# Kernel optimization log

Hardware: AMD Instinct MI355X
Metric: run time of the kernel (lower is better)

## Reference

```python
import jax, jax.numpy as jnp
import numpy as np

EPS = 1e-5  # torch BatchNorm default eps


def _bn(x, gamma, beta, axes):
    # training-mode batch norm over `axes` (channel axis is 1), biased variance as in torch
    mean = x.mean(axis=axes, keepdims=True)
    var = x.var(axis=axes, keepdims=True)
    shp = [1] * x.ndim
    shp[1] = -1
    return gamma.reshape(shp) * (x - mean) * jax.lax.rsqrt(var + EPS) + beta.reshape(shp)


def setup_inputs() -> dict:
    key = jax.random.key(0)
    k0, k1, k2 = jax.random.split(key, 3)
    B, C, H, W = 4, 64, 128, 128
    OP2 = 128      # out_planes * 2
    HEAD = 8       # head_dim
    HP = OP2 // HEAD  # head_planes = 16
    return {
        "x": jax.random.normal(k0, (B, C, H, W), jnp.float32),
        "w_qkv": jax.random.normal(k1, (OP2, C), jnp.float32) / np.sqrt(C).astype(np.float32),
        "gamma1": jnp.ones((OP2,), jnp.float32),
        "beta1": jnp.zeros((OP2,), jnp.float32),
        "pos_relative": jax.random.normal(k2, (HP, 2 * H - 1), jnp.float32) / np.sqrt(C).astype(np.float32),
        "gate_qr": jnp.array([0.1], jnp.float32),
        "gate_kr": jnp.array([0.1], jnp.float32),
        "gate_v_pos": jnp.array([0.1], jnp.float32),
        "gate_v": jnp.array([1.0], jnp.float32),
        "gamma_att": jnp.ones((3 * HEAD,), jnp.float32),
        "beta_att": jnp.zeros((3 * HEAD,), jnp.float32),
        "gamma_v": jnp.ones((2 * HEAD,), jnp.float32),
        "beta_v": jnp.zeros((2 * HEAD,), jnp.float32),
    }


def reference(x, w_qkv, gamma1, beta1, pos_relative, gate_qr, gate_kr,
              gate_v_pos, gate_v, gamma_att, beta_att, gamma_v, beta_v):
    b, c, H, W = x.shape
    # h_w='h': permute [0,3,1,2] -> (b, W, c, H), fuse (b, W)
    xp = jnp.transpose(x, (0, 3, 1, 2)).reshape(b * W, c, H)  # [N, c, H]
    # to_qkv: 1x1 Conv1d (no bias) + ReLU + BatchNorm1d (training mode)
    y = jax.nn.relu(jnp.einsum('oc,ncl->nol', w_qkv, xp))      # [N, 2*out_planes, H]
    y = _bn(y, gamma1, beta1, (0, 2))

    head_dim = gamma_att.shape[0] // 3
    hp = y.shape[1] // head_dim          # head_planes
    qk_dim = hp // 4
    v_dim = hp // 2
    qkv = y.reshape(-1, head_dim, hp, H)  # [N, head_dim, head_planes, H]
    q = qkv[:, :, :qk_dim]
    k = qkv[:, :, qk_dim:2 * qk_dim]
    v = qkv[:, :, 2 * qk_dim:]

    # relative-position gather: pos_relative[:, q_idx - k_idx + H - 1] -> [head_planes, H, H]
    rel = jnp.arange(H)[:, None] - jnp.arange(H)[None, :] + H - 1
    qk_pos = pos_relative[:, rel]
    q_pos = qk_pos[:qk_dim]
    k_pos = qk_pos[qk_dim:2 * qk_dim]
    v_pos = qk_pos[2 * qk_dim:]

    qk = jnp.einsum('nhcp,nhci->nhpi', q, k)                 # [N, head_dim, H, H]
    qr = jnp.einsum('nhcp,cpi->nhpi', q, q_pos) * gate_qr
    kr = jnp.einsum('nhcp,cpi->nhpi', k, k_pos) * gate_kr

    att = _bn(jnp.concatenate([qk, qr, kr], axis=1), gamma_att, beta_att, (0, 2, 3))
    att = att.reshape(-1, 3, head_dim, H, H).sum(axis=1)
    att = jax.nn.softmax(att, axis=-1)

    att_v = jnp.einsum('nhpi,nhci->nhcp', att, v * gate_v)          # [N, head_dim, v_dim, H]
    att_vp = jnp.einsum('nhpi,cpi->nhcp', att, v_pos * gate_v_pos)

    z = _bn(jnp.concatenate([att_v, att_vp], axis=1), gamma_v, beta_v, (0, 2, 3))
    z = z.reshape(b, W, 2, head_dim * v_dim, H).sum(axis=2)  # [b, W, out_planes, H]
    # h_w='h': permute [0,2,3,1] -> (b, out_planes, H, W)
    return jnp.transpose(z, (0, 2, 3, 1))
```

## Files before the change

### kernel.cpp

```cpp
#include <hip/hip_runtime.h>
#include <hip/hip_fp16.h>

#define EPS 1e-5f



typedef _Float16 half2_t __attribute__((ext_vector_type(2)));

__device__ __constant__ int pair_c [10] = {0,0,0,0,1,1,1,2,2,3};
__device__ __constant__ int pair_cp[10] = {0,1,2,3,1,2,3,2,3,3};
__device__ __constant__ int s_base[6] = {512, 536, 520, 544, 528, 552};

__device__ inline float fdot2(half2_t a, half2_t b, float c) {
#if __has_builtin(__builtin_amdgcn_fdot2)
  return __builtin_amdgcn_fdot2(a, b, c, false);
#else
  return c + (float)a[0] * (float)b[0] + (float)a[1] * (float)b[1];
#endif
}
__device__ inline half2_t bch2(unsigned u) {
  union { unsigned u; half2_t h; } x; x.u = u; return x.h;
}
__device__ inline unsigned packf2(float a, float b) {
  half2_t h; h[0] = (_Float16)a; h[1] = (_Float16)b;
  union { unsigned u; half2_t h; } x; x.h = h; return x.u;
}

__global__ __launch_bounds__(256) void k1_gemm(
    const float* __restrict__ x, const float* __restrict__ wq,
    float* __restrict__ y1, float* __restrict__ Pbuf)
{
  __shared__ float xs[64][132];
  const int b = blockIdx.x >> 7, l = blockIdx.x & 127;
  const int tid = threadIdx.x;
  const float* xp = x + (size_t)b * 1048576 + (size_t)l * 128;
  for (int idx = tid; idx < 8192; idx += 256) {
    int c = idx >> 7, wv = idx & 127;
    xs[c][wv] = xp[c * 16384 + wv];
  }
  __syncthreads();
  const int ty = tid >> 4, tx = tid & 15;
  const int o0 = ty * 8, w0 = tx * 4;
  float acc[8][8];
#pragma unroll
  for (int u = 0; u < 8; ++u)
#pragma unroll
    for (int v = 0; v < 8; ++v) acc[u][v] = 0.f;

  for (int c4 = 0; c4 < 64; c4 += 4) {
    float wr[8][4];
#pragma unroll
    for (int u = 0; u < 8; ++u)
      *(float4*)&wr[u][0] = *(const float4*)&wq[(o0 + u) * 64 + c4];
#pragma unroll
    for (int dc = 0; dc < 4; ++dc) {
      float4 xa = *(const float4*)&xs[c4 + dc][w0];
      float4 xb = *(const float4*)&xs[c4 + dc][w0 + 64];
#pragma unroll
      for (int u = 0; u < 8; ++u) {
        float wv = wr[u][dc];
        acc[u][0] += wv * xa.x; acc[u][1] += wv * xa.y;
        acc[u][2] += wv * xa.z; acc[u][3] += wv * xa.w;
        acc[u][4] += wv * xb.x; acc[u][5] += wv * xb.y;
        acc[u][6] += wv * xb.z; acc[u][7] += wv * xb.w;
      }
    }
  }
  float* y1p = y1 + (size_t)(b * 128 + l) * 16384;
#pragma unroll
  for (int u = 0; u < 8; ++u) {
#pragma unroll
    for (int v = 0; v < 8; ++v) acc[u][v] = fmaxf(acc[u][v], 0.f);
    float4 r0 = make_float4(acc[u][0], acc[u][1], acc[u][2], acc[u][3]);
    float4 r1 = make_float4(acc[u][4], acc[u][5], acc[u][6], acc[u][7]);
    *(float4*)&y1p[(o0 + u) * 128 + w0] = r0;
    *(float4*)&y1p[(o0 + u) * 128 + w0 + 64] = r1;
    float s  = acc[u][0] + acc[u][1] + acc[u][2] + acc[u][3]
             + acc[u][4] + acc[u][5] + acc[u][6] + acc[u][7];
    float ss = acc[u][0]*acc[u][0] + acc[u][1]*acc[u][1] + acc[u][2]*acc[u][2]
             + acc[u][3]*acc[u][3] + acc[u][4]*acc[u][4] + acc[u][5]*acc[u][5]
             + acc[u][6]*acc[u][6] + acc[u][7]*acc[u][7];
#pragma unroll
    for (int off = 1; off < 16; off <<= 1) {
      s  += __shfl_xor(s, off);
      ss += __shfl_xor(ss, off);
    }
    if (tx == 0) {
      Pbuf[blockIdx.x * 256 + o0 + u] = s;
      Pbuf[blockIdx.x * 256 + 128 + o0 + u] = ss;
    }
  }
}

__global__ __launch_bounds__(64) void k2_bn1(
    const float* __restrict__ Pbuf, float* __restrict__ S,
    const float* __restrict__ g1, const float* __restrict__ b1)
{
  const int t = blockIdx.x;
  const int lane = threadIdx.x;
  float s1 = 0.f, s2 = 0.f;
#pragma unroll
  for (int m = 0; m < 8; ++m) {
    int blk = lane + 64 * m;
    s1 += Pbuf[blk * 256 + t];
    s2 += Pbuf[blk * 256 + 128 + t];
  }
#pragma unroll
  for (int off = 1; off < 64; off <<= 1) {
    s1 += __shfl_xor(s1, off);
    s2 += __shfl_xor(s2, off);
  }
  if (lane == 0) {
    const float inv = 1.f / 65536.f;
    float m = s1 * inv;
    float var = s2 * inv - m * m;
    float sc = g1[t] * rsqrtf(var + EPS);
    S[256 + t] = sc;
    S[384 + t] = b1[t] - m * sc;
  }
}

__global__ __launch_bounds__(256) void k_tr(
    const float* __restrict__ y1, const float* __restrict__ S,
    unsigned* __restrict__ y2h)
{
  __shared__ _Float16 th[2][64][134];
  const int s = blockIdx.x & 63, b = blockIdx.x >> 6;
  const int h = s >> 3, slot = s & 7;
  const int o0 = 2 * s, o1 = 2 * s + 1;
  const float sc0 = S[256 + o0], sh0 = S[384 + o0];
  const float sc1 = S[256 + o1], sh1 = S[384 + o1];
  const int tid = threadIdx.x;
  for (int lh = 0; lh < 2; ++lh) {
    const int l0 = lh * 64;
    for (int idx = tid; idx < 8192; idx += 256) {
      int ll = idx >> 7, w = idx & 127;
      size_t base = ((size_t)(b * 128 + l0 + ll) * 128) * 128 + w;
      float v0 = y1[base + (size_t)o0 * 128];
      float v1 = y1[base + (size_t)o1 * 128];
      th[0][ll][w] = (_Float16)(v0 * sc0 + sh0);
      th[1][ll][w] = (_Float16)(v1 * sc1 + sh1);
    }
    __syncthreads();
    for (int idx = tid; idx < 8192; idx += 256) {
      int w = idx >> 6, ll = idx & 63;
      unsigned pk;
      { half2_t hh; hh[0] = th[0][ll][w]; hh[1] = th[1][ll][w];
        union { unsigned u; half2_t h; } xx; xx.h = hh; pk = xx.u; }
      y2h[((size_t)((b * 128 + w) * 8 + h) * 8 + slot) * 128 + l0 + ll] = pk;
    }
    __syncthreads();
  }
}

__global__ __launch_bounds__(128) void k0_pos(const float* __restrict__ pos,
                                              float* __restrict__ PT,
                                              unsigned* __restrict__ pos_h)
{
  const int blk = blockIdx.x, tid = threadIdx.x;
  if (blk == 28) {
    for (int u = tid; u < 255; u += 128) {
#pragma unroll
      for (int s = 0; s < 12; ++s) {
        unsigned val = 0;
        if (s < 8) val = packf2(pos[(2 * s) * 255 + u], pos[(2 * s + 1) * 255 + u]);
        pos_h[u * 12 + s] = val;
      }
    }
    return;
  }
  __shared__ float r0[255], r1[255];
  int rowA, rowB, out;
  bool prod;
  if (blk < 4)       { rowA = blk;                 rowB = rowA;               out = blk * 128;              prod = false; }
  else if (blk < 14) { int m = blk - 4;  rowA = pair_c[m];     rowB = pair_cp[m];     out = 1024 + m * 128; prod = true; }
  else if (blk < 18) { rowA = 4 + (blk - 14);      rowB = rowA;               out = 512 + (blk - 14) * 128; prod = false; }
  else               { int m = blk - 18; rowA = 4 + pair_c[m]; rowB = 4 + pair_cp[m]; out = 2304 + m * 128; prod = true; }
  for (int u = tid; u < 255; u += 128) {
    r0[u] = pos[rowA * 255 + u];
    r1[u] = pos[rowB * 255 + u];
  }
  __syncthreads();
  float s = 0.f;
  if (prod) {
    for (int d = 0; d < 128; ++d) s += r0[tid + d] * r1[tid + d];
  } else {
    for (int d = 0; d < 128; ++d) s += r0[tid + d];
  }
  PT[out + tid] = s;
}

__global__ __launch_bounds__(256) void k3_stats(
    const unsigned* __restrict__ y2h, const float* __restrict__ PT,
    float* __restrict__ Pb3)
{
  const int W = blockIdx.x * 4 + (threadIdx.x >> 6);
  const int lane = threadIdx.x & 63;
  const int h = W & 7;
  const int n0 = (W >> 3) * 8;
  float Pq[4][2], Pk[4][2], Wq[10][2], Wk[10][2];
#pragma unroll
  for (int c = 0; c < 4; ++c) {
    Pq[c][0] = PT[c * 128 + lane];        Pq[c][1] = PT[c * 128 + 64 + lane];
    Pk[c][0] = PT[512 + c * 128 + lane];  Pk[c][1] = PT[512 + c * 128 + 64 + lane];
  }
#pragma unroll
  for (int m = 0; m < 10; ++m) {
    Wq[m][0] = PT[1024 + m * 128 + lane]; Wq[m][1] = PT[1024 + m * 128 + 64 + lane];
    Wk[m][0] = PT[2304 + m * 128 + lane]; Wk[m][1] = PT[2304 + m * 128 + 64 + lane];
  }
  float acc_qk = 0, acc_qkss = 0, acc_qr = 0, acc_qrss = 0, acc_kr = 0, acc_krss = 0;
  for (int t = 0; t < 8; ++t) {
    const unsigned* yb = y2h + (size_t)((n0 + t) * 8 + h) * 1024;
    float q[4][2], k[4][2];
#pragma unroll
    for (int pl = 0; pl < 2; ++pl) {
      half2_t ha = bch2(yb[pl * 128 + lane]);
      half2_t hb = bch2(yb[pl * 128 + 64 + lane]);
      q[2 * pl][0] = (float)ha[0]; q[2 * pl + 1][0] = (float)ha[1];
      q[2 * pl][1] = (float)hb[0]; q[2 * pl + 1][1] = (float)hb[1];
      half2_t hc = bch2(yb[(2 + pl) * 128 + lane]);
      half2_t hd = bch2(yb[(2 + pl) * 128 + 64 + lane]);
      k[2 * pl][0] = (float)hc[0]; k[2 * pl + 1][0] = (float)hc[1];
      k[2 * pl][1] = (float)hd[0]; k[2 * pl + 1][1] = (float)hd[1];
    }
#pragma unroll
    for (int c = 0; c < 4; ++c) {
      acc_qr += q[c][0] * Pq[c][0] + q[c][1] * Pq[c][1];
      acc_kr += k[c][0] * Pk[c][0] + k[c][1] * Pk[c][1];
    }
#pragma unroll
    for (int m = 0; m < 10; ++m) {
      int c = pair_c[m], cp = pair_cp[m];
      float mult = (c == cp) ? 1.f : 2.f;
      acc_qrss += mult * (q[c][0] * q[cp][0] * Wq[m][0] + q[c][1] * q[cp][1] * Wq[m][1]);
      acc_krss += mult * (k[c][0] * k[cp][0] * Wk[m][0] + k[c][1] * k[cp][1] * Wk[m][1]);
    }
    float vals[28];
#pragma unroll
    for (int c = 0; c < 4; ++c) {
      vals[c]     = q[c][0] + q[c][1];
      vals[4 + c] = k[c][0] + k[c][1];
    }
#pragma unroll
    for (int m = 0; m < 10; ++m) {
      int c = pair_c[m], cp = pair_cp[m];
      vals[8 + m]  = q[c][0] * q[cp][0] + q[c][1] * q[cp][1];
      vals[18 + m] = k[c][0] * k[cp][0] + k[c][1] * k[cp][1];
    }
#pragma unroll
    for (int v = 0; v < 28; ++v) {
      float tv = vals[v];
#pragma unroll
      for (int off = 1; off < 64; off <<= 1) tv += __shfl_xor(tv, off);
      vals[v] = tv;
    }
    float qk = 0, qkss = 0;
#pragma unroll
    for (int c = 0; c < 4; ++c) qk += vals[c] * vals[4 + c];
#pragma unroll
    for (int m = 0; m < 10; ++m) {
      float mult = (pair_c[m] == pair_cp[m]) ? 1.f : 2.f;
      qkss += mult * vals[8 + m] * vals[18 + m];
    }
    acc_qk += qk; acc_qkss += qkss;
  }
  float lin[4] = {acc_qr, acc_qrss, acc_kr, acc_krss};
#pragma unroll
  for (int v = 0; v < 4; ++v) {
    float tv = lin[v];
#pragma unroll
    for (int off = 1; off < 64; off <<= 1) tv += __shfl_xor(tv, off);
    lin[v] = tv;
  }
  if (lane == 0) {
    float* o = Pb3 + W * 6;
    o[0] = acc_qk; o[1] = acc_qkss;
    o[2] = lin[0]; o[3] = lin[1]; o[4] = lin[2]; o[5] = lin[3];
  }
}

__global__ __launch_bounds__(64) void k3_red(
    const float* __restrict__ Pb3, float* __restrict__ S)
{
  const int h = blockIdx.x / 6, k = blockIdx.x % 6;
  const int g = threadIdx.x;
  float v = Pb3[(h + 8 * g) * 6 + k];
#pragma unroll
  for (int off = 1; off < 64; off <<= 1) v += __shfl_xor(v, off);
  if (g == 0) S[s_base[k] + h] = v;
}

__global__ void k4_att(float* __restrict__ S, const float* __restrict__ ga,
                       const float* __restrict__ ba,
                       const float* __restrict__ gqr, const float* __restrict__ gkr)
{
  int h = threadIdx.x;
  if (h >= 8) return;
  const float inv = 1.f / 8388608.f;
  float gates[3] = {1.f, gqr[0], gkr[0]};
  float csum = 0.f;
#pragma unroll
  for (int g = 0; g < 3; ++g) {
    float mr = S[512 + g * 8 + h] * inv;
    float er = S[536 + g * 8 + h] * inv;
    float gt = gates[g];
    float mean = gt * mr;
    float var = gt * gt * er - mean * mean;
    float sc = ga[g * 8 + h] * rsqrtf(var + EPS);
    S[560 + g * 8 + h] = gt * sc;
    csum += ba[g * 8 + h] - mean * sc;
  }
  S[584 + h] = csum;
}

__global__ __launch_bounds__(512, 6) void k5_apply(
    const unsigned* __restrict__ y2h, const unsigned* __restrict__ pos_h,
    float* __restrict__ S, _Float16* __restrict__ av, _Float16* __restrict__ avp,
    const float* __restrict__ gv_p, const float* __restrict__ gvp_p,
    float* __restrict__ Vbuf)
{
  __shared__ __align__(16) unsigned qkv_s[128][8];
  __shared__ __align__(16) unsigned posm[255][12];
  __shared__ float red[8][4];
  const int h = blockIdx.x & 7, n = blockIdx.x >> 3;
  const int tid = threadIdx.x;
  const unsigned* yb = y2h + (size_t)(n * 8 + h) * 1024;
  unsigned* qf = (unsigned*)qkv_s;
  for (int m = tid; m < 1024; m += 512)
    qf[m] = yb[(m & 7) * 128 + (m >> 3)];
  unsigned* pf = (unsigned*)posm;
  for (int m = tid; m < 3060; m += 512) pf[m] = pos_h[m];
  __syncthreads();

  const int p = tid >> 2, isub = tid & 3;
  uint4 qk4 = *(const uint4*)&qkv_s[p][0];
  const half2_t q01 = bch2(qk4.x), q23 = bch2(qk4.y);
  const half2_t k01 = bch2(qk4.z), k23 = bch2(qk4.w);
  const float C0 = S[560 + h], C1 = S[568 + h], C2 = S[576 + h], C3v = S[584 + h];

  float sum = 0.f;
  float accv[8], accvp[8];
#pragma unroll
  for (int c = 0; c < 8; ++c) { accv[c] = 0.f; accvp[c] = 0.f; }

#pragma unroll 4
  for (int j = 0; j < 32; ++j) {
    int i = isub + 4 * j;
    int u = p - i + 127;
    uint2 kt  = *(const uint2*)&qkv_s[i][2];
    uint4 qkp = *(const uint4*)&posm[u][0];
    float aa = fdot2(q23, bch2(kt.y),  fdot2(q01, bch2(kt.x),  0.f));
    float bq = fdot2(q23, bch2(qkp.y), fdot2(q01, bch2(qkp.x), 0.f));
    float ck = fdot2(k23, bch2(qkp.w), fdot2(k01, bch2(qkp.z), 0.f));
    float s = aa * C0 + bq * C1 + ck * C2 + C3v;
    float e = __expf(s - 9.f);
    sum += e;
    uint4 vv = *(const uint4*)&qkv_s[i][4];
    uint4 vp = *(const uint4*)&posm[u][4];
    half2_t v0 = bch2(vv.x), v1 = bch2(vv.y), v2 = bch2(vv.z), v3 = bch2(vv.w);
    half2_t w0 = bch2(vp.x), w1 = bch2(vp.y), w2 = bch2(vp.z), w3 = bch2(vp.w);
    accv[0] += e * (float)v0[0]; accv[1] += e * (float)v0[1];
    accv[2] += e * (float)v1[0]; accv[3] += e * (float)v1[1];
    accv[4] += e * (float)v2[0]; accv[5] += e * (float)v2[1];
    accv[6] += e * (float)v3[0]; accv[7] += e * (float)v3[1];
    accvp[0] += e * (float)w0[0]; accvp[1] += e * (float)w0[1];
    accvp[2] += e * (float)w1[0]; accvp[3] += e * (float)w1[1];
    accvp[4] += e * (float)w2[0]; accvp[5] += e * (float)w2[1];
    accvp[6] += e * (float)w3[0]; accvp[7] += e * (float)w3[1];
  }
  sum += __shfl_xor(sum, 1);
  sum += __shfl_xor(sum, 2);
#pragma unroll
  for (int c = 0; c < 8; ++c) {
    accv[c]  += __shfl_xor(accv[c], 1);  accv[c]  += __shfl_xor(accv[c], 2);
    accvp[c] += __shfl_xor(accvp[c], 1); accvp[c] += __shfl_xor(accvp[c], 2);
  }

  float sv = 0, ssv = 0, svp = 0, ssvp = 0;
  if (isub == 0) {
    const float fv = gv_p[0] / sum, fp2 = gvp_p[0] / sum;
    size_t base = ((size_t)(n * 8 + h) * 8) * 128 + p;
#pragma unroll
    for (int c = 0; c < 8; ++c) {
      float x1 = accv[c] * fv;
      float x2 = accvp[c] * fp2;
      av [base + c * 128] = (_Float16)x1;
      avp[base + c * 128] = (_Float16)x2;
      sv += x1; ssv += x1 * x1; svp += x2; ssvp += x2 * x2;
    }
  }
  float vals[4] = {sv, ssv, svp, ssvp};
#pragma unroll
  for (int kk = 0; kk < 4; ++kk) {
    float v = vals[kk];
#pragma unroll
    for (int off = 1; off < 64; off <<= 1) v += __shfl_xor(v, off);
    vals[kk] = v;
  }
  const int wid = tid >> 6, lane = tid & 63;
  if (lane == 0) {
#pragma unroll
    for (int kk = 0; kk < 4; ++kk) red[wid][kk] = vals[kk];
  }
  __syncthreads();
  if (tid == 0) {
    float t0 = 0, t1 = 0, t2 = 0, t3 = 0;
#pragma unroll
    for (int w = 0; w < 8; ++w) {
      t0 += red[w][0]; t1 += red[w][1]; t2 += red[w][2]; t3 += red[w][3];
    }
    float* o = Vbuf + (size_t)blockIdx.x * 4;
    o[0] = t0; o[1] = t1; o[2] = t2; o[3] = t3;
  }
}

__global__ __launch_bounds__(64) void k6_red(
    const float* __restrict__ Vbuf, float* __restrict__ S)
{
  const int k = blockIdx.x >> 3, h = blockIdx.x & 7;
  const int lane = threadIdx.x;
  float v = 0.f;
#pragma unroll
  for (int j = 0; j < 8; ++j) {
    int n = lane + 64 * j;
    v += Vbuf[(size_t)(n * 8 + h) * 4 + k];
  }
#pragma unroll
  for (int off = 1; off < 64; off <<= 1) v += __shfl_xor(v, off);
  if (lane == 0) {
    const int dst[4] = {592, 608, 600, 616};
    S[dst[k] + h] = v;
  }
}

__global__ void k6_v(float* __restrict__ S, const float* __restrict__ gv,
                     const float* __restrict__ bv)
{
  int h = threadIdx.x;
  if (h >= 8) return;
  const float inv = 1.f / 524288.f;
  float m = S[592 + h] * inv;
  float var = S[608 + h] * inv - m * m;
  float sc = gv[h] * rsqrtf(var + EPS);
  S[624 + h] = sc;
  S[632 + h] = bv[h] - m * sc;
  m = S[600 + h] * inv;
  var = S[616 + h] * inv - m * m;
  sc = gv[8 + h] * rsqrtf(var + EPS);
  S[640 + h] = sc;
  S[648 + h] = bv[8 + h] - m * sc;
}

__global__ __launch_bounds__(256) void k7_out(
    const _Float16* __restrict__ av, const _Float16* __restrict__ avp,
    const float* __restrict__ S, float* __restrict__ out)
{
  __shared__ float tile[64][129];
  const int wt = blockIdx.x & 1;
  const int d  = (blockIdx.x >> 1) & 63;
  const int b  = blockIdx.x >> 7;
  const int h = d >> 3, c = d & 7;
  const float scv = S[624 + h], shv = S[632 + h];
  const float scp = S[640 + h], shp = S[648 + h];
  const int tid = threadIdx.x;
  for (int idx = tid; idx < 8192; idx += 256) {
    int wl = idx >> 7, p = idx & 127;
    int n = b * 128 + wt * 64 + wl;
    size_t base = (((size_t)n * 8 + h) * 8 + c) * 128 + p;
    tile[wl][p] = (float)av[base] * scv + shv + (float)avp[base] * scp + shp;
  }
  __syncthreads();
  for (int idx = tid; idx < 8192; idx += 256) {
    int p = idx >> 6, wl = idx & 63;
    out[(((size_t)b * 64 + d) * 128 + p) * 128 + wt * 64 + wl] = tile[wl][p];
  }
}

extern "C" void kernel_launch(void* const* d_in, const int* in_sizes, int n_in,
                              void* d_out, int out_size, void* d_ws, size_t ws_size,
                              hipStream_t stream)
{
  const float* x   = (const float*)d_in[0];
  const float* wq  = (const float*)d_in[1];
  const float* g1  = (const float*)d_in[2];
  const float* b1  = (const float*)d_in[3];
  const float* pos = (const float*)d_in[4];
  const float* gqr = (const float*)d_in[5];
  const float* gkr = (const float*)d_in[6];
  const float* gvp = (const float*)d_in[7];
  const float* gv  = (const float*)d_in[8];
  const float* ga  = (const float*)d_in[9];
  const float* ba  = (const float*)d_in[10];
  const float* gv2 = (const float*)d_in[11];
  const float* bv2 = (const float*)d_in[12];

  float* ws = (float*)d_ws;
  float*    y1    = ws;
  _Float16* av    = (_Float16*)ws;
  _Float16* avp   = (_Float16*)ws + 4194304;
  float*    Pb3   = ws + 4200000;
  float*    Vbuf  = ws + 4250000;
  float*    Pbuf  = ws + 8388608;
  unsigned* y2h   = (unsigned*)(ws + 8388608);
  float*    S     = ws + 16777216;
  unsigned* pos_h = (unsigned*)(ws + 16778240);
  float*    PT    = ws + 16781312;
  float*    out   = (float*)d_out;

  hipMemsetAsync(S, 0, 1024 * sizeof(float), stream);
  k0_pos<<<29, 128, 0, stream>>>(pos, PT, pos_h);
  k1_gemm<<<512, 256, 0, stream>>>(x, wq, y1, Pbuf);
  k2_bn1<<<128, 64, 0, stream>>>(Pbuf, S, g1, b1);
  k_tr<<<256, 256, 0, stream>>>(y1, S, y2h);
  k3_stats<<<128, 256, 0, stream>>>(y2h, PT, Pb3);
  k3_red<<<48, 64, 0, stream>>>(Pb3, S);
  k4_att<<<1, 64, 0, stream>>>(S, ga, ba, gqr, gkr);
  k5_apply<<<4096, 512, 0, stream>>>(y2h, pos_h, S, av, avp, gv, gvp, Vbuf);
  k6_red<<<32, 64, 0, stream>>>(Vbuf, S);
  k6_v<<<1, 64, 0, stream>>>(S, gv2, bv2);
  k7_out<<<512, 256, 0, stream>>>(av, avp, S, out);
}
```

Measured before the change: 218.4 us.

## Store conv output in fp16, fuse small reductions, pack softmax-V dots with online max

The 1x1-conv output is now written as fp16 instead of fp32, which halves traffic between the GEMM and the transpose kernel. The tiny reduction and BN-coefficient kernels are merged (k3_red+k4_att into kR1, k6_red+k6_v into kR2) and the memset is dropped, which removes several launches. The attention-apply kernel now processes key pairs with packed fp16 exp weights and fdot2 for the V and V-pos accumulation. It uses an online running max in place of a fixed offset, with a pre-transposed V tile and a precomputed reversed v_pos table. This lowers ALU and LDS work, at the cost of extra fp16 rounding of y1 and of the exp weights.

```diff
diff --git a/kernel.cpp b/kernel.cpp
--- a/kernel.cpp
+++ b/kernel.cpp
@@ -9,7 +9,6 @@
 
 __device__ __constant__ int pair_c [10] = {0,0,0,0,1,1,1,2,2,3};
 __device__ __constant__ int pair_cp[10] = {0,1,2,3,1,2,3,2,3,3};
-__device__ __constant__ int s_base[6] = {512, 536, 520, 544, 528, 552};
 
 __device__ inline float fdot2(half2_t a, half2_t b, float c) {
 #if __has_builtin(__builtin_amdgcn_fdot2)
@@ -28,7 +27,7 @@
 
 __global__ __launch_bounds__(256) void k1_gemm(
     const float* __restrict__ x, const float* __restrict__ wq,
-    float* __restrict__ y1, float* __restrict__ Pbuf)
+    _Float16* __restrict__ y1h, float* __restrict__ Pbuf)
 {
   __shared__ float xs[64][132];
   const int b = blockIdx.x >> 7, l = blockIdx.x & 127;
@@ -66,15 +65,16 @@
       }
     }
   }
-  float* y1p = y1 + (size_t)(b * 128 + l) * 16384;
+  _Float16* y1p = y1h + (size_t)(b * 128 + l) * 16384;
 #pragma unroll
   for (int u = 0; u < 8; ++u) {
 #pragma unroll
     for (int v = 0; v < 8; ++v) acc[u][v] = fmaxf(acc[u][v], 0.f);
-    float4 r0 = make_float4(acc[u][0], acc[u][1], acc[u][2], acc[u][3]);
-    float4 r1 = make_float4(acc[u][4], acc[u][5], acc[u][6], acc[u][7]);
-    *(float4*)&y1p[(o0 + u) * 128 + w0] = r0;
-    *(float4*)&y1p[(o0 + u) * 128 + w0 + 64] = r1;
+    uint2 pa, pb;
+    pa.x = packf2(acc[u][0], acc[u][1]); pa.y = packf2(acc[u][2], acc[u][3]);
+    pb.x = packf2(acc[u][4], acc[u][5]); pb.y = packf2(acc[u][6], acc[u][7]);
+    *(uint2*)&y1p[(o0 + u) * 128 + w0] = pa;
+    *(uint2*)&y1p[(o0 + u) * 128 + w0 + 64] = pb;
     float s  = acc[u][0] + acc[u][1] + acc[u][2] + acc[u][3]
              + acc[u][4] + acc[u][5] + acc[u][6] + acc[u][7];
     float ss = acc[u][0]*acc[u][0] + acc[u][1]*acc[u][1] + acc[u][2]*acc[u][2]
@@ -121,7 +121,7 @@
 }
 
 __global__ __launch_bounds__(256) void k_tr(
-    const float* __restrict__ y1, const float* __restrict__ S,
+    const _Float16* __restrict__ y1h, const float* __restrict__ S,
     unsigned* __restrict__ y2h)
 {
   __shared__ _Float16 th[2][64][134];
@@ -133,13 +133,16 @@
   const int tid = threadIdx.x;
   for (int lh = 0; lh < 2; ++lh) {
     const int l0 = lh * 64;
-    for (int idx = tid; idx < 8192; idx += 256) {
-      int ll = idx >> 7, w = idx & 127;
-      size_t base = ((size_t)(b * 128 + l0 + ll) * 128) * 128 + w;
-      float v0 = y1[base + (size_t)o0 * 128];
-      float v1 = y1[base + (size_t)o1 * 128];
-      th[0][ll][w] = (_Float16)(v0 * sc0 + sh0);
-      th[1][ll][w] = (_Float16)(v1 * sc1 + sh1);
+    for (int idx = tid; idx < 4096; idx += 256) {
+      int ll = idx >> 6, wp = idx & 63;
+      size_t base = ((size_t)(b * 128 + l0 + ll) * 128) * 128 + 2 * wp;
+      unsigned a0 = *(const unsigned*)&y1h[base + (size_t)o0 * 128];
+      unsigned a1 = *(const unsigned*)&y1h[base + (size_t)o1 * 128];
+      half2_t ha = bch2(a0), hb = bch2(a1);
+      *(unsigned*)&th[0][ll][2 * wp] =
+          packf2((float)ha[0] * sc0 + sh0, (float)ha[1] * sc0 + sh0);
+      *(unsigned*)&th[1][ll][2 * wp] =
+          packf2((float)hb[0] * sc1 + sh1, (float)hb[1] * sc1 + sh1);
     }
     __syncthreads();
     for (int idx = tid; idx < 8192; idx += 256) {
@@ -155,17 +158,30 @@
 
 __global__ __launch_bounds__(128) void k0_pos(const float* __restrict__ pos,
                                               float* __restrict__ PT,
-                                              unsigned* __restrict__ pos_h)
+                                              unsigned* __restrict__ pos_h,
+                                              unsigned* __restrict__ vpxg)
 {
   const int blk = blockIdx.x, tid = threadIdx.x;
   if (blk == 28) {
     for (int u = tid; u < 255; u += 128) {
 #pragma unroll
-      for (int s = 0; s < 12; ++s) {
-        unsigned val = 0;
-        if (s < 8) val = packf2(pos[(2 * s) * 255 + u], pos[(2 * s + 1) * 255 + u]);
-        pos_h[u * 12 + s] = val;
+      for (int s = 0; s < 4; ++s)
+        pos_h[u * 4 + s] = packf2(pos[(2 * s) * 255 + u], pos[(2 * s + 1) * 255 + u]);
+    }
+    return;
+  }
+  if (blk == 29) {
+    for (int m = tid; m < 3072; m += 128) {
+      int sel = m / 1536, rem = m % 1536, rp = rem / 12, c = rem % 12;
+      unsigned val = 0;
+      if (c < 8) {
+        int ua = (sel ? 254 : 253) - 2 * rp;
+        int ub = ua - 1;
+        float fa = (ua >= 0) ? pos[(8 + c) * 255 + ua] : 0.f;
+        float fb = (ub >= 0) ? pos[(8 + c) * 255 + ub] : 0.f;
+        val = packf2(fa, fb);
       }
+      vpxg[m] = val;
     }
     return;
   }
@@ -280,94 +296,148 @@
   }
 }
 
-__global__ __launch_bounds__(64) void k3_red(
-    const float* __restrict__ Pb3, float* __restrict__ S)
-{
-  const int h = blockIdx.x / 6, k = blockIdx.x % 6;
-  const int g = threadIdx.x;
-  float v = Pb3[(h + 8 * g) * 6 + k];
-#pragma unroll
-  for (int off = 1; off < 64; off <<= 1) v += __shfl_xor(v, off);
-  if (g == 0) S[s_base[k] + h] = v;
-}
-
-__global__ void k4_att(float* __restrict__ S, const float* __restrict__ ga,
-                       const float* __restrict__ ba,
-                       const float* __restrict__ gqr, const float* __restrict__ gkr)
-{
-  int h = threadIdx.x;
-  if (h >= 8) return;
-  const float inv = 1.f / 8388608.f;
-  float gates[3] = {1.f, gqr[0], gkr[0]};
-  float csum = 0.f;
-#pragma unroll
-  for (int g = 0; g < 3; ++g) {
-    float mr = S[512 + g * 8 + h] * inv;
-    float er = S[536 + g * 8 + h] * inv;
-    float gt = gates[g];
-    float mean = gt * mr;
-    float var = gt * gt * er - mean * mean;
-    float sc = ga[g * 8 + h] * rsqrtf(var + EPS);
-    S[560 + g * 8 + h] = gt * sc;
-    csum += ba[g * 8 + h] - mean * sc;
-  }
-  S[584 + h] = csum;
+__global__ __launch_bounds__(64) void kR1(
+    const float* __restrict__ Pb3, float* __restrict__ S,
+    const float* __restrict__ ga, const float* __restrict__ ba,
+    const float* __restrict__ gqr, const float* __restrict__ gkr)
+{
+  __shared__ float sums[48];
+  const int t = threadIdx.x;
+  if (t < 48) {
+    int h = t / 6, k = t % 6;
+    float v = 0.f;
+    for (int g = 0; g < 64; ++g) v += Pb3[(h + 8 * g) * 6 + k];
+    sums[t] = v;
+  }
+  __syncthreads();
+  if (t < 8) {
+    const int h = t;
+    const float inv = 1.f / 8388608.f;
+    float gates[3] = {1.f, gqr[0], gkr[0]};
+    float csum = 0.f;
+#pragma unroll
+    for (int g = 0; g < 3; ++g) {
+      float mr = sums[h * 6 + 2 * g] * inv;
+      float er = sums[h * 6 + 2 * g + 1] * inv;
+      float gt = gates[g];
+      float mean = gt * mr;
+      float var = gt * gt * er - mean * mean;
+      float sc = ga[g * 8 + h] * rsqrtf(var + EPS);
+      S[560 + g * 8 + h] = gt * sc;
+      csum += ba[g * 8 + h] - mean * sc;
+    }
+    S[584 + h] = csum;
+  }
 }
 
 __global__ __launch_bounds__(512, 6) void k5_apply(
     const unsigned* __restrict__ y2h, const unsigned* __restrict__ pos_h,
+    const unsigned* __restrict__ vpxg,
     float* __restrict__ S, _Float16* __restrict__ av, _Float16* __restrict__ avp,
     const float* __restrict__ gv_p, const float* __restrict__ gvp_p,
     float* __restrict__ Vbuf)
 {
-  __shared__ __align__(16) unsigned qkv_s[128][8];
-  __shared__ __align__(16) unsigned posm[255][12];
+  __shared__ __align__(16) unsigned qkv_s[128][4];
+  __shared__ __align__(16) unsigned posm[255][4];
+  __shared__ __align__(16) unsigned vt[64][8];
+  __shared__ __align__(16) unsigned vpx[2][128][12];
   __shared__ float red[8][4];
   const int h = blockIdx.x & 7, n = blockIdx.x >> 3;
   const int tid = threadIdx.x;
   const unsigned* yb = y2h + (size_t)(n * 8 + h) * 1024;
-  unsigned* qf = (unsigned*)qkv_s;
-  for (int m = tid; m < 1024; m += 512)
-    qf[m] = yb[(m & 7) * 128 + (m >> 3)];
-  unsigned* pf = (unsigned*)posm;
-  for (int m = tid; m < 3060; m += 512) pf[m] = pos_h[m];
+  {
+    int l = tid >> 2, s = tid & 3;
+    qkv_s[l][s] = yb[s * 128 + l];
+  }
+  {
+    unsigned* pf = (unsigned*)posm;
+    for (int m = tid; m < 1020; m += 512) pf[m] = pos_h[m];
+  }
+  {
+    unsigned* pf = (unsigned*)vpx;
+    for (int m = tid; m < 3072; m += 512) pf[m] = vpxg[m];
+  }
+  if (tid < 256) {
+    int s = tid & 3, jp = tid >> 2;
+    unsigned a0 = yb[(4 + s) * 128 + 2 * jp];
+    unsigned a1 = yb[(4 + s) * 128 + 2 * jp + 1];
+    vt[jp][2 * s]     = (a0 & 0xffffu) | (a1 << 16);
+    vt[jp][2 * s + 1] = (a0 >> 16) | (a1 & 0xffff0000u);
+  }
   __syncthreads();
 
   const int p = tid >> 2, isub = tid & 3;
-  uint4 qk4 = *(const uint4*)&qkv_s[p][0];
-  const half2_t q01 = bch2(qk4.x), q23 = bch2(qk4.y);
-  const half2_t k01 = bch2(qk4.z), k23 = bch2(qk4.w);
+  uint2 qk2 = *(const uint2*)&qkv_s[p][0];
+  uint2 kown = *(const uint2*)&qkv_s[p][2];
+  const half2_t q01 = bch2(qk2.x), q23 = bch2(qk2.y);
+  const half2_t k01o = bch2(kown.x), k23o = bch2(kown.y);
   const float C0 = S[560 + h], C1 = S[568 + h], C2 = S[576 + h], C3v = S[584 + h];
-
+  const unsigned* vprow = &vpx[p & 1][63 - (p >> 1)][0];
+
+  float mcur = -1e30f;
   float sum = 0.f;
   float accv[8], accvp[8];
 #pragma unroll
   for (int c = 0; c < 8; ++c) { accv[c] = 0.f; accvp[c] = 0.f; }
 
 #pragma unroll 4
-  for (int j = 0; j < 32; ++j) {
-    int i = isub + 4 * j;
-    int u = p - i + 127;
-    uint2 kt  = *(const uint2*)&qkv_s[i][2];
-    uint4 qkp = *(const uint4*)&posm[u][0];
-    float aa = fdot2(q23, bch2(kt.y),  fdot2(q01, bch2(kt.x),  0.f));
-    float bq = fdot2(q23, bch2(qkp.y), fdot2(q01, bch2(qkp.x), 0.f));
-    float ck = fdot2(k23, bch2(qkp.w), fdot2(k01, bch2(qkp.z), 0.f));
-    float s = aa * C0 + bq * C1 + ck * C2 + C3v;
-    float e = __expf(s - 9.f);
-    sum += e;
-    uint4 vv = *(const uint4*)&qkv_s[i][4];
-    uint4 vp = *(const uint4*)&posm[u][4];
-    half2_t v0 = bch2(vv.x), v1 = bch2(vv.y), v2 = bch2(vv.z), v3 = bch2(vv.w);
-    half2_t w0 = bch2(vp.x), w1 = bch2(vp.y), w2 = bch2(vp.z), w3 = bch2(vp.w);
-    accv[0] += e * (float)v0[0]; accv[1] += e * (float)v0[1];
-    accv[2] += e * (float)v1[0]; accv[3] += e * (float)v1[1];
-    accv[4] += e * (float)v2[0]; accv[5] += e * (float)v2[1];
-    accv[6] += e * (float)v3[0]; accv[7] += e * (float)v3[1];
-    accvp[0] += e * (float)w0[0]; accvp[1] += e * (float)w0[1];
-    accvp[2] += e * (float)w1[0]; accvp[3] += e * (float)w1[1];
-    accvp[4] += e * (float)w2[0]; accvp[5] += e * (float)w2[1];
-    accvp[6] += e * (float)w3[0]; accvp[7] += e * (float)w3[1];
+  for (int j = 0; j < 16; ++j) {
+    const int jp = isub + 4 * j;
+    const int i0 = 2 * jp;
+    const int u0 = p - i0 + 127;
+    uint2 ka = *(const uint2*)&qkv_s[i0][2];
+    uint2 kb = *(const uint2*)&qkv_s[i0 + 1][2];
+    uint4 pa = *(const uint4*)&posm[u0][0];
+    uint4 pb = *(const uint4*)&posm[u0 - 1][0];
+    float aa0 = fdot2(q23, bch2(ka.y), fdot2(q01, bch2(ka.x), 0.f));
+    float bq0 = fdot2(q23, bch2(pa.y), fdot2(q01, bch2(pa.x), 0.f));
+    float ckA = fdot2(k23o, bch2(pa.w), fdot2(k01o, bch2(pa.z), 0.f));
+    float aa1 = fdot2(q23, bch2(kb.y), fdot2(q01, bch2(kb.x), 0.f));
+    float bq1 = fdot2(q23, bch2(pb.y), fdot2(q01, bch2(pb.x), 0.f));
+    float ckB = fdot2(k23o, bch2(pb.w), fdot2(k01o, bch2(pb.z), 0.f));
+    float s0 = aa0 * C0 + bq0 * C1 + ckA * C2 + C3v;
+    float s1 = aa1 * C0 + bq1 * C1 + ckB * C2 + C3v;
+    float mp = fmaxf(s0, s1);
+    if (mp > mcur) {
+      float r = __expf(mcur - mp);
+      mcur = mp;
+      sum *= r;
+#pragma unroll
+      for (int c = 0; c < 8; ++c) { accv[c] *= r; accvp[c] *= r; }
+    }
+    float e0 = __expf(s0 - mcur);
+    float e1 = __expf(s1 - mcur);
+    sum += e0 + e1;
+    const half2_t e2 = bch2(packf2(e0, e1));
+    uint4 va = *(const uint4*)&vt[jp][0];
+    uint4 vb = *(const uint4*)&vt[jp][4];
+    const unsigned* wr = vprow + jp * 12;
+    uint4 wa = *(const uint4*)wr;
+    uint4 wb = *(const uint4*)(wr + 4);
+    accv[0] = fdot2(e2, bch2(va.x), accv[0]);
+    accv[1] = fdot2(e2, bch2(va.y), accv[1]);
+    accv[2] = fdot2(e2, bch2(va.z), accv[2]);
+    accv[3] = fdot2(e2, bch2(va.w), accv[3]);
+    accv[4] = fdot2(e2, bch2(vb.x), accv[4]);
+    accv[5] = fdot2(e2, bch2(vb.y), accv[5]);
+    accv[6] = fdot2(e2, bch2(vb.z), accv[6]);
+    accv[7] = fdot2(e2, bch2(vb.w), accv[7]);
+    accvp[0] = fdot2(e2, bch2(wa.x), accvp[0]);
+    accvp[1] = fdot2(e2, bch2(wa.y), accvp[1]);
+    accvp[2] = fdot2(e2, bch2(wa.z), accvp[2]);
+    accvp[3] = fdot2(e2, bch2(wa.w), accvp[3]);
+    accvp[4] = fdot2(e2, bch2(wb.x), accvp[4]);
+    accvp[5] = fdot2(e2, bch2(wb.y), accvp[5]);
+    accvp[6] = fdot2(e2, bch2(wb.z), accvp[6]);
+    accvp[7] = fdot2(e2, bch2(wb.w), accvp[7]);
+  }
+  float M = fmaxf(mcur, __shfl_xor(mcur, 1));
+  M = fmaxf(M, __shfl_xor(M, 2));
+  {
+    float r = __expf(mcur - M);
+    sum *= r;
+#pragma unroll
+    for (int c = 0; c < 8; ++c) { accv[c] *= r; accvp[c] *= r; }
   }
   sum += __shfl_xor(sum, 1);
   sum += __shfl_xor(sum, 2);
@@ -415,41 +485,44 @@
   }
 }
 
-__global__ __launch_bounds__(64) void k6_red(
-    const float* __restrict__ Vbuf, float* __restrict__ S)
-{
-  const int k = blockIdx.x >> 3, h = blockIdx.x & 7;
-  const int lane = threadIdx.x;
+__global__ __launch_bounds__(512) void kR2(
+    const float* __restrict__ Vbuf, float* __restrict__ S,
+    const float* __restrict__ gv, const float* __restrict__ bv)
+{
+  __shared__ float part[32][17];
+  const int t = threadIdx.x;
+  const int col = t >> 4, sub = t & 15;
+  const int k = col >> 3, h = col & 7;
   float v = 0.f;
-#pragma unroll
-  for (int j = 0; j < 8; ++j) {
-    int n = lane + 64 * j;
+  for (int m = 0; m < 32; ++m) {
+    int n = sub + 16 * m;
     v += Vbuf[(size_t)(n * 8 + h) * 4 + k];
   }
-#pragma unroll
-  for (int off = 1; off < 64; off <<= 1) v += __shfl_xor(v, off);
-  if (lane == 0) {
-    const int dst[4] = {592, 608, 600, 616};
-    S[dst[k] + h] = v;
-  }
-}
-
-__global__ void k6_v(float* __restrict__ S, const float* __restrict__ gv,
-                     const float* __restrict__ bv)
-{
-  int h = threadIdx.x;
-  if (h >= 8) return;
-  const float inv = 1.f / 524288.f;
-  float m = S[592 + h] * inv;
-  float var = S[608 + h] * inv - m * m;
-  float sc = gv[h] * rsqrtf(var + EPS);
-  S[624 + h] = sc;
-  S[632 + h] = bv[h] - m * sc;
-  m = S[600 + h] * inv;
-  var = S[616 + h] * inv - m * m;
-  sc = gv[8 + h] * rsqrtf(var + EPS);
-  S[640 + h] = sc;
-  S[648 + h] = bv[8 + h] - m * sc;
+  part[col][sub] = v;
+  __syncthreads();
+  if (t < 32) {
+    float s = 0.f;
+#pragma unroll
+    for (int j = 0; j < 16; ++j) s += part[t][j];
+    part[t][16] = s;
+  }
+  __syncthreads();
+  if (t < 8) {
+    const int hh = t;
+    const float inv = 1.f / 524288.f;
+    float m1 = part[0 * 8 + hh][16] * inv;
+    float e1 = part[1 * 8 + hh][16] * inv;
+    float var = e1 - m1 * m1;
+    float sc = gv[hh] * rsqrtf(var + EPS);
+    S[624 + hh] = sc;
+    S[632 + hh] = bv[hh] - m1 * sc;
+    float m2 = part[2 * 8 + hh][16] * inv;
+    float e2 = part[3 * 8 + hh][16] * inv;
+    var = e2 - m2 * m2;
+    sc = gv[8 + hh] * rsqrtf(var + EPS);
+    S[640 + hh] = sc;
+    S[648 + hh] = bv[8 + hh] - m2 * sc;
+  }
 }
 
 __global__ __launch_bounds__(256) void k7_out(
@@ -465,15 +538,15 @@
   const float scp = S[640 + h], shp = S[648 + h];
   const int tid = threadIdx.x;
   for (int idx = tid; idx < 8192; idx += 256) {
-    int wl = idx >> 7, p = idx & 127;
+    int wl = idx >> 7, pp = idx & 127;
     int n = b * 128 + wt * 64 + wl;
-    size_t base = (((size_t)n * 8 + h) * 8 + c) * 128 + p;
-    tile[wl][p] = (float)av[base] * scv + shv + (float)avp[base] * scp + shp;
+    size_t base = (((size_t)n * 8 + h) * 8 + c) * 128 + pp;
+    tile[wl][pp] = (float)av[base] * scv + shv + (float)avp[base] * scp + shp;
   }
   __syncthreads();
   for (int idx = tid; idx < 8192; idx += 256) {
-    int p = idx >> 6, wl = idx & 63;
-    out[(((size_t)b * 64 + d) * 128 + p) * 128 + wt * 64 + wl] = tile[wl][p];
+    int pp = idx >> 6, wl = idx & 63;
+    out[(((size_t)b * 64 + d) * 128 + pp) * 128 + wt * 64 + wl] = tile[wl][pp];
   }
 }
 
@@ -496,7 +569,7 @@
   const float* bv2 = (const float*)d_in[12];
 
   float* ws = (float*)d_ws;
-  float*    y1    = ws;
+  _Float16* y1h   = (_Float16*)ws;
   _Float16* av    = (_Float16*)ws;
   _Float16* avp   = (_Float16*)ws + 4194304;
   float*    Pb3   = ws + 4200000;
@@ -506,18 +579,16 @@
   float*    S     = ws + 16777216;
   unsigned* pos_h = (unsigned*)(ws + 16778240);
   float*    PT    = ws + 16781312;
+  unsigned* vpxg  = (unsigned*)(ws + 16785000);
   float*    out   = (float*)d_out;
 
-  hipMemsetAsync(S, 0, 1024 * sizeof(float), stream);
-  k0_pos<<<29, 128, 0, stream>>>(pos, PT, pos_h);
-  k1_gemm<<<512, 256, 0, stream>>>(x, wq, y1, Pbuf);
+  k0_pos<<<30, 128, 0, stream>>>(pos, PT, pos_h, vpxg);
+  k1_gemm<<<512, 256, 0, stream>>>(x, wq, y1h, Pbuf);
   k2_bn1<<<128, 64, 0, stream>>>(Pbuf, S, g1, b1);
-  k_tr<<<256, 256, 0, stream>>>(y1, S, y2h);
+  k_tr<<<256, 256, 0, stream>>>(y1h, S, y2h);
   k3_stats<<<128, 256, 0, stream>>>(y2h, PT, Pb3);
-  k3_red<<<48, 64, 0, stream>>>(Pb3, S);
-  k4_att<<<1, 64, 0, stream>>>(S, ga, ba, gqr, gkr);
-  k5_apply<<<4096, 512, 0, stream>>>(y2h, pos_h, S, av, avp, gv, gvp, Vbuf);
-  k6_red<<<32, 64, 0, stream>>>(Vbuf, S);
-  k6_v<<<1, 64, 0, stream>>>(S, gv2, bv2);
+  kR1<<<1, 64, 0, stream>>>(Pb3, S, ga, ba, gqr, gkr);
+  k5_apply<<<4096, 512, 0, stream>>>(y2h, pos_h, vpxg, S, av, avp, gv, gvp, Vbuf);
+  kR2<<<1, 512, 0, stream>>>(Vbuf, S, gv2, bv2);
   k7_out<<<512, 256, 0, stream>>>(av, avp, S, out);
 }
```

New measurement: 215.7 us. No clear change (-1.2%).
